# Performance work log

Measured on AMD Instinct MI355X. Metric: run time of the kernel, lower is better.

The kernel has to match this reference:

```python
import jax, jax.numpy as jnp
import numpy as np

NUM_HEADS = 8


def _proj(W, b, x):
    # x: [B, C, N] channel-wise 1x1 conv == matmul over channels
    return jnp.einsum('oc,bcn->bon', W, x) + b[None, :, None]


def setup_inputs() -> dict:
    key = jax.random.key(0)
    ks = jax.random.split(key, 8)
    B, C, H, W = 4, 512, 24, 24
    inp = {
        'feat0': jax.random.normal(ks[0], (B, C, H, W), jnp.float32),
        'feat1': jax.random.normal(ks[1], (B, C, H, W), jnp.float32),
        'feat2': jax.random.normal(ks[2], (B, C, H, W), jnp.float32),
        'Wq': jax.random.normal(ks[3], (C, C), jnp.float32) * 0.02,
        'bq': jnp.zeros((C,), jnp.float32),
        'Wk': jax.random.normal(ks[4], (C, C), jnp.float32) * 0.02,
        'bk': jnp.zeros((C,), jnp.float32),
        'Wv': jax.random.normal(ks[5], (C, C), jnp.float32) * 0.02,
        'bv': jnp.zeros((C,), jnp.float32),
        'Wo': jax.random.normal(ks[6], (C, C), jnp.float32) * 0.02,
        'bo': jnp.zeros((C,), jnp.float32),
    }
    return inp


def reference(feat0, feat1, feat2, Wq, bq, Wk, bk, Wv, bv, Wo, bo):
    feats = [feat0, feat1, feat2]
    B, C, H, W = feat0.shape
    h = NUM_HEADS
    d = C // h
    scale = d ** -0.5

    # Precompute K/V once per feature (the torch loop redundantly recomputes them;
    # the math is identical).
    flat = [f.reshape(B, C, H * W) for f in feats]
    K = jnp.concatenate([_proj(Wk, bk, x).reshape(B, h, d, -1) for x in flat], axis=-1)  # [B,h,d,KV]
    V = jnp.concatenate([_proj(Wv, bv, x).reshape(B, h, d, -1) for x in flat], axis=-1)  # [B,h,d,KV]

    outs = []
    for feat, x in zip(feats, flat):
        q = _proj(Wq, bq, x).reshape(B, h, d, H * W)  # [B,h,d,N]
        attn = jax.nn.softmax(jnp.einsum('bhdn,bhdm->bhnm', q, K) * scale, axis=-1)
        out = jnp.einsum('bhnm,bhdm->bhdn', attn, V).reshape(B, C, H * W)
        out = _proj(Wo, bo, out).reshape(B, C, H, W)
        outs.append(feat + out)
    return tuple(outs)
```

## Files before the change

kernel.cpp:

```cpp
#include <hip/hip_runtime.h>


using bf16x8 = __attribute__((ext_vector_type(8))) short;
using f32x4  = __attribute__((ext_vector_type(4))) float;
using f32x16 = __attribute__((ext_vector_type(16))) float;
using u32x4  = __attribute__((ext_vector_type(4))) unsigned int;
using u16x4  = __attribute__((ext_vector_type(4))) unsigned short;
using u16x8  = __attribute__((ext_vector_type(8))) unsigned short;

#define MFMA16(a, b, c) __builtin_amdgcn_mfma_f32_16x16x32_bf16((a), (b), (c), 0, 0, 0)
#define MFMA32(a, b, c) __builtin_amdgcn_mfma_f32_32x32x16_bf16((a), (b), (c), 0, 0, 0)

__device__ __forceinline__ unsigned short f2bf(float f) {
  unsigned int u = __float_as_uint(f);
  return (unsigned short)((u + 0x7fffu + ((u >> 16) & 1u)) >> 16);
}

__device__ __forceinline__ f32x16 zero16() {
  f32x16 z;
#pragma unroll
  for (int i = 0; i < 16; ++i) z[i] = 0.f;
  return z;
}

__global__ __launch_bounds__(256) void k_cvt_w(
    const float* __restrict__ Wq, const float* __restrict__ Wk,
    const float* __restrict__ Wv, const float* __restrict__ Wo,
    unsigned short* __restrict__ Wf) {
  int i   = blockIdx.x * 256 + threadIdx.x;
  int idx = i * 4;
  int p   = idx >> 18;
  int rem = idx & 262143;
  int o = rem >> 9, c0 = rem & 511;
  const float* s = p == 0 ? Wq : p == 1 ? Wk : p == 2 ? Wv : Wo;
  f32x4 v = *(const f32x4*)(s + rem);
  u16x4 pk;
  pk[0] = f2bf(v[0]); pk[1] = f2bf(v[1]); pk[2] = f2bf(v[2]); pk[3] = f2bf(v[3]);
  int mt = o >> 6, fr = (o & 63) >> 4, lr = o & 15;
  int ks = c0 >> 5, lg = (c0 & 31) >> 3, j0 = c0 & 7;
  size_t off = (size_t)((((p * 8 + mt) * 16 + ks) * 4 + fr)) * 512 +
               (lg * 16 + lr) * 8 + j0;
  *(u16x4*)(Wf + off) = pk;
}

__global__ __launch_bounds__(256) void k_pack_xt(
    const float* __restrict__ f0, const float* __restrict__ f1,
    const float* __restrict__ f2, unsigned short* __restrict__ Xf) {
  const int nt = blockIdx.x;
  const int ct = blockIdx.y;
  const int z  = blockIdx.z;
  const int b = z / 3, f = z % 3;
  const int t = threadIdx.x;
  const float* src = (f == 0 ? f0 : f == 1 ? f1 : f2) + b * (512 * 576);

  __shared__ unsigned short tile[64][65];
#pragma unroll
  for (int i = 0; i < 16; ++i) {
    int idx = i * 256 + t;
    int cc = idx >> 6, nn = idx & 63;
    tile[cc][nn] = f2bf(src[(ct * 64 + cc) * 576 + nt * 64 + nn]);
  }
  __syncthreads();
  const int ntw = f * 9 + nt;
#pragma unroll
  for (int i = 0; i < 4; ++i) {
    int slot = i * 256 + t;
    int nn = slot >> 4, cq = slot & 15;
    int cl = cq * 4;
    int c  = ct * 64 + cl;
    int fc = nn >> 4, lr = nn & 15;
    int ks = c >> 5, lg = (c & 31) >> 3, j0 = c & 7;
    u16x4 pk;
    pk[0] = tile[cl][nn]; pk[1] = tile[cl + 1][nn];
    pk[2] = tile[cl + 2][nn]; pk[3] = tile[cl + 3][nn];
    size_t off = (size_t)((((b * 27 + ntw) * 16 + ks) * 4 + fc)) * 512 +
                 (lg * 16 + lr) * 8 + j0;
    *(u16x4*)(Xf + off) = pk;
  }
}

__global__ __launch_bounds__(256) void k_gemm_qkv(
    const unsigned short* __restrict__ Wf, const unsigned short* __restrict__ Xf,
    const float* __restrict__ bq, const float* __restrict__ bk,
    const float* __restrict__ bv,
    unsigned short* __restrict__ Qf, unsigned short* __restrict__ Kf,
    unsigned short* __restrict__ Vf) {
  const int id = blockIdx.x;
  const int xcd = id & 7, s = id >> 3;
  const int b = xcd >> 1, par = xcd & 1;
  const int p = s / 27, bx = (s % 27) * 2 + par;
  const int t = threadIdx.x, w = t >> 6, l = t & 63, lg = l >> 4, lr = l & 15;
  const int wid = bx * 4 + w;
  const int mt = wid / 27, ntw = wid % 27;
  const unsigned short* A = Wf + (size_t)(p * 8 + mt) * 16 * 2048 + l * 8;
  const unsigned short* B = Xf + (size_t)(b * 27 + ntw) * 16 * 2048 + l * 8;

  f32x4 acc[4][4];
#pragma unroll
  for (int fr = 0; fr < 4; ++fr)
#pragma unroll
    for (int fc = 0; fc < 4; ++fc) acc[fr][fc] = (f32x4){0.f, 0.f, 0.f, 0.f};

#pragma unroll 2
  for (int ks = 0; ks < 16; ++ks) {
    bf16x8 af[4], bfv[4];
#pragma unroll
    for (int fr = 0; fr < 4; ++fr)
      af[fr] = *(const bf16x8*)(A + ks * 2048 + fr * 512);
#pragma unroll
    for (int fc = 0; fc < 4; ++fc)
      bfv[fc] = *(const bf16x8*)(B + ks * 2048 + fc * 512);
#pragma unroll
    for (int fr = 0; fr < 4; ++fr)
#pragma unroll
      for (int fc = 0; fc < 4; ++fc)
        acc[fr][fc] = MFMA16(af[fr], bfv[fc], acc[fr][fc]);
  }

  const float* bias = p == 0 ? bq : p == 1 ? bk : bv;
  const int bh = b * 8 + mt;
#pragma unroll
  for (int fr = 0; fr < 4; ++fr) {
    f32x4 b4 = *(const f32x4*)(bias + mt * 64 + fr * 16 + lg * 4);
#pragma unroll
    for (int fc = 0; fc < 4; ++fc) {
      int ck = ntw * 2 + (fc >> 1);
      if (p < 2) {
        unsigned short* outF = (p == 0) ? Qf : Kf;
        u16x4 pk;
#pragma unroll
        for (int r = 0; r < 4; ++r) pk[r] = f2bf(acc[fr][fc][r] + b4[r]);
        size_t off = ((size_t)bh * 54 + ck) * 2048 + fr * 512 +
                     ((lg >> 1) * 32 + (fc & 1) * 16 + lr) * 8 + (lg & 1) * 4;
        *(u16x4*)(outF + off) = pk;
      } else {
        size_t base = ((size_t)bh * 54 + ck) * 2048 +
                      ((fr >> 1) * 2 + (fc & 1)) * 512 +
                      (((lr >> 3) & 1) * 32 + (fr & 1) * 16 + lg * 4) * 8 +
                      (lr & 7);
#pragma unroll
        for (int r = 0; r < 4; ++r)
          Vf[base + r * 8] = f2bf(acc[fr][fc][r] + b4[r]);
      }
    }
  }
}

__device__ __forceinline__ void attn_tile(const f32x16& s, float& lsum,
                                          f32x16 oacc[2],
                                          const bf16x8 vb[4], int hi) {
  float pv[16];
  float a0 = 0.f, a1 = 0.f;
#pragma unroll
  for (int r = 0; r < 16; ++r) {
    float e;
    asm("v_exp_f32 %0, %1" : "=v"(e) : "v"(s[r] * 0.18033688f));
    pv[r] = e;
    if (r & 1) a1 += e; else a0 += e;
  }
  lsum += a0 + a1;
  unsigned int W[8];
#pragma unroll
  for (int u = 0; u < 8; ++u)
    asm("v_cvt_pk_bf16_f32 %0, %1, %2"
        : "=v"(W[u]) : "v"(pv[2 * u]), "v"(pv[2 * u + 1]));
  unsigned int fw[2][4];
#pragma unroll
  for (int kf = 0; kf < 2; ++kf)
#pragma unroll
    for (int wd = 0; wd < 2; ++wd) {
      unsigned int lo  = W[4 * kf + wd];
      unsigned int hw  = W[4 * kf + 2 + wd];
      unsigned int pub = hi ? lo : hw;
      unsigned int rcv = (unsigned int)__shfl_xor((int)pub, 32, 64);
      fw[kf][wd]     = hi ? rcv : lo;
      fw[kf][2 + wd] = hi ? hw : rcv;
    }
#pragma unroll
  for (int kf2 = 0; kf2 < 2; ++kf2) {
    u32x4 fv;
    fv[0] = fw[kf2][0]; fv[1] = fw[kf2][1];
    fv[2] = fw[kf2][2]; fv[3] = fw[kf2][3];
    bf16x8 pa = __builtin_bit_cast(bf16x8, fv);
#pragma unroll
    for (int dt = 0; dt < 2; ++dt)
      oacc[dt] = MFMA32(pa, vb[dt * 2 + kf2], oacc[dt]);
  }
}

__global__ __launch_bounds__(256) void k_attn(
    const unsigned short* __restrict__ Qf, const unsigned short* __restrict__ Kf,
    const unsigned short* __restrict__ Vf, unsigned short* __restrict__ Of) {
  const int id = blockIdx.x;
  const int xcd = id & 7, slot = id >> 3;
  const int bh = xcd * 4 + (slot / 54);
  const int qt = slot % 54;
  const int b = bh >> 3, h = bh & 7;
  const int t = threadIdx.x, w = t >> 6, l = t & 63;
  const int lr = l & 31, hi = l >> 5;

  __shared__ float Obuf[4][32][68];
  __shared__ float Lbuf[4][32];

  const unsigned short* Qb = Qf + ((size_t)bh * 54 + qt) * 2048 + l * 8;
  bf16x8 bq[4];
#pragma unroll
  for (int kf = 0; kf < 4; ++kf) bq[kf] = *(const bf16x8*)(Qb + kf * 512);

  f32x16 oacc[2];
  oacc[0] = zero16(); oacc[1] = zero16();
  float ls = 0.f;

  const unsigned short* Kb = Kf + (size_t)bh * 54 * 2048 + l * 8;
  const unsigned short* Vb = Vf + (size_t)bh * 54 * 2048 + l * 8;

  for (int ck = w; ck < 54; ck += 4) {
    const unsigned short* kc = Kb + ck * 2048;
    const unsigned short* vc = Vb + ck * 2048;
    bf16x8 ak[4], vb[4];
#pragma unroll
    for (int kf = 0; kf < 4; ++kf) ak[kf] = *(const bf16x8*)(kc + kf * 512);
#pragma unroll
    for (int i = 0; i < 4; ++i) vb[i] = *(const bf16x8*)(vc + i * 512);

    f32x16 s0 = zero16();
#pragma unroll
    for (int kf = 0; kf < 4; ++kf) s0 = MFMA32(ak[kf], bq[kf], s0);
    attn_tile(s0, ls, oacc, vb, hi);
  }

  float lt = ls + __shfl_xor(ls, 32, 64);
  if (l < 32) Lbuf[w][lr] = lt;
#pragma unroll
  for (int dt = 0; dt < 2; ++dt)
#pragma unroll
    for (int r = 0; r < 16; ++r)
      Obuf[w][(r & 3) + 8 * (r >> 2) + 4 * hi][dt * 32 + lr] = oacc[dt][r];
  __syncthreads();

  const int n = t >> 3, d0 = (t & 7) * 8;
  float ltot = Lbuf[0][n] + Lbuf[1][n] + Lbuf[2][n] + Lbuf[3][n];
  float linv = 1.0f / ltot;
  u16x8 o8;
#pragma unroll
  for (int i = 0; i < 8; ++i) {
    float ov = Obuf[0][n][d0 + i] + Obuf[1][n][d0 + i] +
               Obuf[2][n][d0 + i] + Obuf[3][n][d0 + i];
    o8[i] = f2bf(ov * linv);
  }
  size_t off = (size_t)((((b * 27 + (qt >> 1)) * 16 + h * 2 + (d0 >> 5)) * 4 +
                         (qt & 1) * 2 + (n >> 4))) * 512 +
               ((d0 >> 3) & 3) * 128 + (n & 15) * 8;
  *(u16x8*)(Of + off) = o8;
}

__global__ __launch_bounds__(256) void k_gemm_out(
    const unsigned short* __restrict__ Wf, const unsigned short* __restrict__ Of,
    const float* __restrict__ bo,
    const float* __restrict__ f0, const float* __restrict__ f1,
    const float* __restrict__ f2, float* __restrict__ out) {
  const int z = blockIdx.z, b = z / 3, f = z % 3;
  const int t = threadIdx.x, w = t >> 6, l = t & 63, lg = l >> 4, lr = l & 15;
  const int wid = blockIdx.x * 4 + w;
  const int mt = wid / 9, ntw = wid % 9;
  const int o0 = mt * 64;
  const unsigned short* A = Wf + (size_t)(3 * 8 + mt) * 16 * 2048 + l * 8;
  const unsigned short* B = Of + (size_t)(b * 27 + f * 9 + ntw) * 16 * 2048 + l * 8;

  f32x4 acc[4][4];
#pragma unroll
  for (int fr = 0; fr < 4; ++fr)
#pragma unroll
    for (int fc = 0; fc < 4; ++fc) acc[fr][fc] = (f32x4){0.f, 0.f, 0.f, 0.f};

#pragma unroll 2
  for (int ks = 0; ks < 16; ++ks) {
    bf16x8 af[4], bfv[4];
#pragma unroll
    for (int fr = 0; fr < 4; ++fr)
      af[fr] = *(const bf16x8*)(A + ks * 2048 + fr * 512);
#pragma unroll
    for (int fc = 0; fc < 4; ++fc)
      bfv[fc] = *(const bf16x8*)(B + ks * 2048 + fc * 512);
#pragma unroll
    for (int fr = 0; fr < 4; ++fr)
#pragma unroll
      for (int fc = 0; fc < 4; ++fc)
        acc[fr][fc] = MFMA16(af[fr], bfv[fc], acc[fr][fc]);
  }

  const float* ft = f == 0 ? f0 : f == 1 ? f1 : f2;
#pragma unroll
  for (int fr = 0; fr < 4; ++fr) {
    f32x4 b4 = *(const f32x4*)(bo + o0 + fr * 16 + lg * 4);
#pragma unroll
    for (int fc = 0; fc < 4; ++fc) {
      int ncol = ntw * 64 + fc * 16 + lr;
#pragma unroll
      for (int r = 0; r < 4; ++r) {
        int o = o0 + fr * 16 + lg * 4 + r;
        out[((f * 4 + b) * 512 + o) * 576 + ncol] =
            acc[fr][fc][r] + b4[r] + ft[(b * 512 + o) * 576 + ncol];
      }
    }
  }
}

extern "C" void kernel_launch(void* const* d_in, const int* in_sizes, int n_in,
                              void* d_out, int out_size, void* d_ws, size_t ws_size,
                              hipStream_t stream) {
  const float* f0 = (const float*)d_in[0];
  const float* f1 = (const float*)d_in[1];
  const float* f2 = (const float*)d_in[2];
  const float* Wq = (const float*)d_in[3];
  const float* bq = (const float*)d_in[4];
  const float* Wk = (const float*)d_in[5];
  const float* bk = (const float*)d_in[6];
  const float* Wv = (const float*)d_in[7];
  const float* bv = (const float*)d_in[8];
  const float* Wo = (const float*)d_in[9];
  const float* bo = (const float*)d_in[10];
  float* out = (float*)d_out;

  char* ws = (char*)d_ws;
  unsigned short* Wf = (unsigned short*)(ws);
  unsigned short* Xf = (unsigned short*)(ws + 2097152);
  unsigned short* Qf = (unsigned short*)(ws + 9175040);
  unsigned short* Kf = (unsigned short*)(ws + 16252928);
  unsigned short* Vf = (unsigned short*)(ws + 23330816);
  unsigned short* Of = Xf;

  k_cvt_w<<<1024, 256, 0, stream>>>(Wq, Wk, Wv, Wo, Wf);
  k_pack_xt<<<dim3(9, 8, 12), 256, 0, stream>>>(f0, f1, f2, Xf);
  k_gemm_qkv<<<dim3(648), 256, 0, stream>>>(Wf, Xf, bq, bk, bv, Qf, Kf, Vf);
  k_attn<<<dim3(1728), 256, 0, stream>>>(Qf, Kf, Vf, Of);
  k_gemm_out<<<dim3(18, 1, 12), 256, 0, stream>>>(Wf, Of, bo, f0, f1, f2, out);
}
```

Measured before the change: 101.7 us.

## Merge weight and input pack kernels; software-pipeline attention QK and PV

Folds the weight-conversion and feature-transpose kernels into one launch, so one kernel launch and its boundary go away. In the attention kernel, the key/value loop is software-pipelined: the next chunk's K/V loads and QK MFMAs are issued while the current chunk's softmax and PV MFMAs run. This hides global-load and MFMA latency, at the cost of more live registers for the double-buffered fragments.

```diff
diff --git a/kernel.cpp b/kernel.cpp
--- a/kernel.cpp
+++ b/kernel.cpp
@@ -23,37 +23,38 @@
   return z;
 }
 
-__global__ __launch_bounds__(256) void k_cvt_w(
+__global__ __launch_bounds__(256) void k_prep(
     const float* __restrict__ Wq, const float* __restrict__ Wk,
     const float* __restrict__ Wv, const float* __restrict__ Wo,
-    unsigned short* __restrict__ Wf) {
-  int i   = blockIdx.x * 256 + threadIdx.x;
-  int idx = i * 4;
-  int p   = idx >> 18;
-  int rem = idx & 262143;
-  int o = rem >> 9, c0 = rem & 511;
-  const float* s = p == 0 ? Wq : p == 1 ? Wk : p == 2 ? Wv : Wo;
-  f32x4 v = *(const f32x4*)(s + rem);
-  u16x4 pk;
-  pk[0] = f2bf(v[0]); pk[1] = f2bf(v[1]); pk[2] = f2bf(v[2]); pk[3] = f2bf(v[3]);
-  int mt = o >> 6, fr = (o & 63) >> 4, lr = o & 15;
-  int ks = c0 >> 5, lg = (c0 & 31) >> 3, j0 = c0 & 7;
-  size_t off = (size_t)((((p * 8 + mt) * 16 + ks) * 4 + fr)) * 512 +
-               (lg * 16 + lr) * 8 + j0;
-  *(u16x4*)(Wf + off) = pk;
-}
-
-__global__ __launch_bounds__(256) void k_pack_xt(
     const float* __restrict__ f0, const float* __restrict__ f1,
-    const float* __restrict__ f2, unsigned short* __restrict__ Xf) {
-  const int nt = blockIdx.x;
-  const int ct = blockIdx.y;
-  const int z  = blockIdx.z;
+    const float* __restrict__ f2,
+    unsigned short* __restrict__ Wf, unsigned short* __restrict__ Xf) {
+  __shared__ unsigned short tile[64][65];
+  const int bid = blockIdx.x;
+  const int t = threadIdx.x;
+  if (bid < 1024) {
+    int idx = (bid * 256 + t) * 4;
+    int p   = idx >> 18;
+    int rem = idx & 262143;
+    int o = rem >> 9, c0 = rem & 511;
+    const float* s = p == 0 ? Wq : p == 1 ? Wk : p == 2 ? Wv : Wo;
+    f32x4 v = *(const f32x4*)(s + rem);
+    u16x4 pk;
+    pk[0] = f2bf(v[0]); pk[1] = f2bf(v[1]); pk[2] = f2bf(v[2]); pk[3] = f2bf(v[3]);
+    int mt = o >> 6, fr = (o & 63) >> 4, lr = o & 15;
+    int ks = c0 >> 5, lg = (c0 & 31) >> 3, j0 = c0 & 7;
+    size_t off = (size_t)((((p * 8 + mt) * 16 + ks) * 4 + fr)) * 512 +
+                 (lg * 16 + lr) * 8 + j0;
+    *(u16x4*)(Wf + off) = pk;
+    return;
+  }
+  const int id = bid - 1024;
+  const int nt = id % 9;
+  const int ct = (id / 9) % 8;
+  const int z  = id / 72;
   const int b = z / 3, f = z % 3;
-  const int t = threadIdx.x;
   const float* src = (f == 0 ? f0 : f == 1 ? f1 : f2) + b * (512 * 576);
 
-  __shared__ unsigned short tile[64][65];
 #pragma unroll
   for (int i = 0; i < 16; ++i) {
     int idx = i * 256 + t;
@@ -146,24 +147,19 @@
   }
 }
 
-__device__ __forceinline__ void attn_tile(const f32x16& s, float& lsum,
-                                          f32x16 oacc[2],
-                                          const bf16x8 vb[4], int hi) {
-  float pv[16];
+__device__ __forceinline__ void softmax_pa(const f32x16& s, float& lsum,
+                                           bf16x8& pa0, bf16x8& pa1, int hi) {
+  unsigned int W[8];
   float a0 = 0.f, a1 = 0.f;
 #pragma unroll
-  for (int r = 0; r < 16; ++r) {
-    float e;
-    asm("v_exp_f32 %0, %1" : "=v"(e) : "v"(s[r] * 0.18033688f));
-    pv[r] = e;
-    if (r & 1) a1 += e; else a0 += e;
+  for (int u = 0; u < 8; ++u) {
+    float e0, e1;
+    asm("v_exp_f32 %0, %1" : "=v"(e0) : "v"(s[2 * u] * 0.18033688f));
+    asm("v_exp_f32 %0, %1" : "=v"(e1) : "v"(s[2 * u + 1] * 0.18033688f));
+    a0 += e0; a1 += e1;
+    asm("v_cvt_pk_bf16_f32 %0, %1, %2" : "=v"(W[u]) : "v"(e0), "v"(e1));
   }
   lsum += a0 + a1;
-  unsigned int W[8];
-#pragma unroll
-  for (int u = 0; u < 8; ++u)
-    asm("v_cvt_pk_bf16_f32 %0, %1, %2"
-        : "=v"(W[u]) : "v"(pv[2 * u]), "v"(pv[2 * u + 1]));
   unsigned int fw[2][4];
 #pragma unroll
   for (int kf = 0; kf < 2; ++kf)
@@ -176,16 +172,11 @@
       fw[kf][wd]     = hi ? rcv : lo;
       fw[kf][2 + wd] = hi ? hw : rcv;
     }
-#pragma unroll
-  for (int kf2 = 0; kf2 < 2; ++kf2) {
-    u32x4 fv;
-    fv[0] = fw[kf2][0]; fv[1] = fw[kf2][1];
-    fv[2] = fw[kf2][2]; fv[3] = fw[kf2][3];
-    bf16x8 pa = __builtin_bit_cast(bf16x8, fv);
-#pragma unroll
-    for (int dt = 0; dt < 2; ++dt)
-      oacc[dt] = MFMA32(pa, vb[dt * 2 + kf2], oacc[dt]);
-  }
+  u32x4 w0, w1;
+  w0[0] = fw[0][0]; w0[1] = fw[0][1]; w0[2] = fw[0][2]; w0[3] = fw[0][3];
+  w1[0] = fw[1][0]; w1[1] = fw[1][1]; w1[2] = fw[1][2]; w1[3] = fw[1][3];
+  pa0 = __builtin_bit_cast(bf16x8, w0);
+  pa1 = __builtin_bit_cast(bf16x8, w1);
 }
 
 __global__ __launch_bounds__(256) void k_attn(
@@ -214,19 +205,53 @@
   const unsigned short* Kb = Kf + (size_t)bh * 54 * 2048 + l * 8;
   const unsigned short* Vb = Vf + (size_t)bh * 54 * 2048 + l * 8;
 
-  for (int ck = w; ck < 54; ck += 4) {
-    const unsigned short* kc = Kb + ck * 2048;
-    const unsigned short* vc = Vb + ck * 2048;
-    bf16x8 ak[4], vb[4];
-#pragma unroll
-    for (int kf = 0; kf < 4; ++kf) ak[kf] = *(const bf16x8*)(kc + kf * 512);
+  bf16x8 ak[4], vb[4];
+  {
+    const unsigned short* kc = Kb + w * 2048;
+    const unsigned short* vc = Vb + w * 2048;
+#pragma unroll
+    for (int i = 0; i < 4; ++i) ak[i] = *(const bf16x8*)(kc + i * 512);
 #pragma unroll
     for (int i = 0; i < 4; ++i) vb[i] = *(const bf16x8*)(vc + i * 512);
-
-    f32x16 s0 = zero16();
-#pragma unroll
-    for (int kf = 0; kf < 4; ++kf) s0 = MFMA32(ak[kf], bq[kf], s0);
-    attn_tile(s0, ls, oacc, vb, hi);
+  }
+  f32x16 sA = zero16();
+#pragma unroll
+  for (int kf = 0; kf < 4; ++kf) sA = MFMA32(ak[kf], bq[kf], sA);
+
+#pragma unroll 1
+  for (int ck = w + 4; ck < 54; ck += 4) {
+    bf16x8 akn[4], vbn[4];
+    const unsigned short* kn = Kb + ck * 2048;
+    const unsigned short* vn = Vb + ck * 2048;
+#pragma unroll
+    for (int i = 0; i < 4; ++i) akn[i] = *(const bf16x8*)(kn + i * 512);
+#pragma unroll
+    for (int i = 0; i < 4; ++i) vbn[i] = *(const bf16x8*)(vn + i * 512);
+
+    bf16x8 pa0, pa1;
+    softmax_pa(sA, ls, pa0, pa1, hi);
+
+    f32x16 sB = zero16();
+#pragma unroll
+    for (int kf = 0; kf < 4; ++kf) sB = MFMA32(akn[kf], bq[kf], sB);
+
+    oacc[0] = MFMA32(pa0, vb[0], oacc[0]);
+    oacc[0] = MFMA32(pa1, vb[1], oacc[0]);
+    oacc[1] = MFMA32(pa0, vb[2], oacc[1]);
+    oacc[1] = MFMA32(pa1, vb[3], oacc[1]);
+
+    sA = sB;
+#pragma unroll
+    for (int i = 0; i < 4; ++i) vb[i] = vbn[i];
+  }
+
+  {
+    bf16x8 pa0, pa1;
+    softmax_pa(sA, ls, pa0, pa1, hi);
+    oacc[0] = MFMA32(pa0, vb[0], oacc[0]);
+    oacc[0] = MFMA32(pa1, vb[1], oacc[0]);
+    oacc[1] = MFMA32(pa0, vb[2], oacc[1]);
+    oacc[1] = MFMA32(pa1, vb[3], oacc[1]);
   }
 
   float lt = ls + __shfl_xor(ls, 32, 64);
@@ -330,8 +355,7 @@
   unsigned short* Vf = (unsigned short*)(ws + 23330816);
   unsigned short* Of = Xf;
 
-  k_cvt_w<<<1024, 256, 0, stream>>>(Wq, Wk, Wv, Wo, Wf);
-  k_pack_xt<<<dim3(9, 8, 12), 256, 0, stream>>>(f0, f1, f2, Xf);
+  k_prep<<<dim3(1888), 256, 0, stream>>>(Wq, Wk, Wv, Wo, f0, f1, f2, Wf, Xf);
   k_gemm_qkv<<<dim3(648), 256, 0, stream>>>(Wf, Xf, bq, bk, bv, Qf, Kf, Vf);
   k_attn<<<dim3(1728), 256, 0, stream>>>(Qf, Kf, Vf, Of);
   k_gemm_out<<<dim3(18, 1, 12), 256, 0, stream>>>(Wf, Of, bo, f0, f1, f2, out);
```

New measurement: 100.1 us. About the same (-1.5%).
